# Kernel optimization log

Measured on AMD Instinct MI355X. Metric: run time of the kernel, lower is better.

Reference implementation:

```python
import jax, jax.numpy as jnp
import numpy as np
import math

B, TSRC, TTGT, DM, DI, H = 2, 2048, 2048, 1024, 1024, 16
DH = DI // H
LN_EPS = 1e-5


def setup_inputs() -> dict:
    key = jax.random.key(0)
    ks = iter(jax.random.split(key, 40))
    def p(*shape):
        return jax.random.normal(next(ks), shape, jnp.float32) * 0.02
    inp = {
        "enc_out_vecs": jax.random.normal(next(ks), (B, TSRC, DM), jnp.float32),
        "output_vecs": jax.random.normal(next(ks), (B, TTGT, DM), jnp.float32),
    }
    for tag in ("dd", "ed"):
        inp["Wq_" + tag] = p(DM, DI); inp["bq_" + tag] = jnp.zeros((DI,), jnp.float32)
        inp["Wk_" + tag] = p(DM, DI); inp["bk_" + tag] = jnp.zeros((DI,), jnp.float32)
        inp["Wv_" + tag] = p(DM, DI); inp["bv_" + tag] = jnp.zeros((DI,), jnp.float32)
        inp["Wo_" + tag] = p(DI, DM); inp["bo_" + tag] = jnp.zeros((DM,), jnp.float32)
        inp["W1_" + tag] = p(DM, 2 * DM); inp["b1_" + tag] = jnp.zeros((2 * DM,), jnp.float32)
        inp["W2_" + tag] = p(2 * DM, DM); inp["b2_" + tag] = jnp.zeros((DM,), jnp.float32)
        inp["g1_" + tag] = jnp.ones((DM,), jnp.float32); inp["be1_" + tag] = jnp.zeros((DM,), jnp.float32)
        inp["g2_" + tag] = jnp.ones((DM,), jnp.float32); inp["be2_" + tag] = jnp.zeros((DM,), jnp.float32)
    return inp


def _ln(x, g, b):
    m = jnp.mean(x, axis=-1, keepdims=True)
    v = jnp.var(x, axis=-1, keepdims=True)
    return (x - m) * jax.lax.rsqrt(v + LN_EPS) * g + b


def _mha(xq, xkv, Wq, bq, Wk, bk, Wv, bv, causal):
    Bb, Tq, _ = xq.shape
    Tk = xkv.shape[1]
    q = (xq @ Wq + bq).reshape(Bb, Tq, H, DH)
    k = (xkv @ Wk + bk).reshape(Bb, Tk, H, DH)
    v = (xkv @ Wv + bv).reshape(Bb, Tk, H, DH)
    s = jnp.einsum("bqhd,bkhd->bhqk", q, k) / math.sqrt(DH)
    if causal:
        mask = jnp.where(jnp.arange(Tk)[None, :] > jnp.arange(Tq)[:, None], -jnp.inf, 0.0)
        s = s + mask
    w = jax.nn.softmax(s, axis=-1)
    return jnp.einsum("bhqk,bkhd->bqhd", w, v).reshape(Bb, Tq, H * DH)


def reference(enc_out_vecs, output_vecs,
              Wq_dd, bq_dd, Wk_dd, bk_dd, Wv_dd, bv_dd, Wo_dd, bo_dd,
              W1_dd, b1_dd, W2_dd, b2_dd, g1_dd, be1_dd, g2_dd, be2_dd,
              Wq_ed, bq_ed, Wk_ed, bk_ed, Wv_ed, bv_ed, Wo_ed, bo_ed,
              W1_ed, b1_ed, W2_ed, b2_ed, g1_ed, be1_ed, g2_ed, be2_ed):
    # masked self-attention over decoder inputs
    x = output_vecs
    a = _mha(x, x, Wq_dd, bq_dd, Wk_dd, bk_dd, Wv_dd, bv_dd, causal=True)
    x = _ln(a @ Wo_dd + bo_dd + x, g1_dd, be1_dd)
    x = _ln(x + jax.nn.relu(x @ W1_dd + b1_dd) @ W2_dd + b2_dd, g2_dd, be2_dd)
    # cross attention against encoder outputs
    a = _mha(x, enc_out_vecs, Wq_ed, bq_ed, Wk_ed, bk_ed, Wv_ed, bv_ed, causal=False)
    x = _ln(a @ Wo_ed + bo_ed + x, g1_ed, be1_ed)
    x = _ln(jax.nn.relu(x @ W1_ed + b1_ed) @ W2_ed + b2_ed + x, g2_ed, be2_ed)
    return x
```

## Files before the change

kernel.cpp:

```cpp
#include <hip/hip_runtime.h>
#include <stdint.h>

#define DEV __device__ __forceinline__
typedef unsigned short u16;
typedef __attribute__((ext_vector_type(8))) short bf16x8;
typedef __attribute__((ext_vector_type(4))) float f32x4;

#define AS1 __attribute__((address_space(1)))
#define AS3 __attribute__((address_space(3)))
#define WAITVM0 asm volatile("s_waitcnt vmcnt(0)" ::: "memory")
#define QSCALE 0.18033688011112042f

DEV u16 f2bf(float f) {
  union { float f; uint32_t u; } x; x.f = f;
  uint32_t r = x.u + 0x7fffu + ((x.u >> 16) & 1u);
  return (u16)(r >> 16);
}

DEV uint32_t cvt_pk_bf16(float a, float b) {
  uint32_t r;
  asm("v_cvt_pk_bf16_f32 %0, %1, %2" : "=v"(r) : "v"(a), "v"(b));
  return r;
}

__global__ __launch_bounds__(256) void k_cvt2(const float* __restrict__ a, const float* __restrict__ bsrc,
                                              u16* __restrict__ oa, u16* __restrict__ ob, int n4) {
  int i = blockIdx.x * blockDim.x + threadIdx.x;
  const float* s;
  u16* o;
  int k;
  if (i < n4) { s = a; o = oa; k = i; }
  else        { s = bsrc; o = ob; k = i - n4; }
  float4 v = reinterpret_cast<const float4*>(s)[k];
  reinterpret_cast<ushort4*>(o)[k] = make_ushort4(f2bf(v.x), f2bf(v.y), f2bf(v.z), f2bf(v.w));
}

struct WTJob { const float* W; u16* WT; int K, M, msh, start; };
struct WTJobs { WTJob j[12]; };

__global__ void k_wT_all(WTJobs jobs) {
  __shared__ float tile[32][33];
  int b = blockIdx.x;
  int i = 0;
#pragma unroll
  for (int t = 1; t < 12; ++t)
    if (b >= jobs.j[t].start) i = t;
  const WTJob J = jobs.j[i];
  int rel = b - J.start;
  int m0 = (rel & ((1 << J.msh) - 1)) << 5;
  int k0 = (rel >> J.msh) << 5;
  int tx = threadIdx.x, ty = threadIdx.y;
#pragma unroll
  for (int q = 0; q < 4; ++q)
    tile[ty + q * 8][tx] = J.W[(size_t)(k0 + ty + q * 8) * J.M + m0 + tx];
  __syncthreads();
#pragma unroll
  for (int q = 0; q < 4; ++q)
    J.WT[(size_t)(m0 + ty + q * 8) * J.K + k0 + tx] = f2bf(tile[tx][ty + q * 8]);
}

template<int R>
DEV void stage_tile(const u16* __restrict__ g, int strideElems, u16* lds, int tid, int wv) {
#pragma unroll
  for (int t = 0; t < R / 32; ++t) {
    int idx = t * 256 + tid;
    int row = idx >> 3;
    int b = (idx & 7) << 4;
    int sb = b ^ ((row & 7) << 4);
    const char* src = (const char*)g + (size_t)row * strideElems * 2 + sb;
    char* dst = (char*)lds + (size_t)(t * 256 + wv * 64) * 16;
    __builtin_amdgcn_global_load_lds((const AS1 void*)src, (AS3 void*)dst, 16, 0, 0);
  }
}

DEV bf16x8 lds_frag(const u16* lds, int row, int kel) {
  int off = row * 128 + ((kel * 2) ^ ((row & 7) << 4));
  return *(const bf16x8*)((const char*)lds + off);
}

template<int JT, int MODE>
__global__ __launch_bounds__(256) void k_gemm(const u16* __restrict__ A, int lda,
                                              const u16* __restrict__ BT,
                                              const float* __restrict__ bias,
                                              void* __restrict__ C, int ldc, int K) {
  constexpr int BN = JT * 32;
  __shared__ __align__(16) u16 A_lds[2][128 * 64];
  __shared__ __align__(16) u16 B_lds[2][BN * 64];
  const int tid = threadIdx.x, lane = tid & 63, wv = tid >> 6;
  const int wm = wv >> 1, wn = wv & 1;
  const int nwg = gridDim.x * gridDim.y;
  const int flat = blockIdx.y * gridDim.x + blockIdx.x;
  const int sw = (flat & 7) * (nwg >> 3) + (flat >> 3);
  const int bx = sw % gridDim.x, by = sw / gridDim.x;
  const int bm0 = by * 128, bn0 = bx * BN;
  const int lr = lane & 15, lk = (lane >> 4) * 8, r0 = (lane >> 4) * 4;

  f32x4 acc[4][JT];
#pragma unroll
  for (int i = 0; i < 4; ++i)
#pragma unroll
    for (int j = 0; j < JT; ++j) acc[i][j] = f32x4{0.f, 0.f, 0.f, 0.f};

  stage_tile<128>(A + (size_t)bm0 * lda, lda, A_lds[0], tid, wv);
  stage_tile<BN>(BT + (size_t)bn0 * K, K, B_lds[0], tid, wv);
  WAITVM0;
  __builtin_amdgcn_s_barrier();

  int cur = 0;
  for (int k0 = 0; k0 < K; k0 += 64) {
    if (k0 + 64 < K) {
      stage_tile<128>(A + (size_t)bm0 * lda + k0 + 64, lda, A_lds[cur ^ 1], tid, wv);
      stage_tile<BN>(BT + (size_t)bn0 * K + k0 + 64, K, B_lds[cur ^ 1], tid, wv);
    }
#pragma unroll
    for (int kk = 0; kk < 2; ++kk) {
      bf16x8 af[4], bfr[JT];
#pragma unroll
      for (int i = 0; i < 4; ++i) af[i] = lds_frag(A_lds[cur], wm * 64 + i * 16 + lr, kk * 32 + lk);
#pragma unroll
      for (int j = 0; j < JT; ++j) bfr[j] = lds_frag(B_lds[cur], wn * (JT * 16) + j * 16 + lr, kk * 32 + lk);
#pragma unroll
      for (int i = 0; i < 4; ++i)
#pragma unroll
        for (int j = 0; j < JT; ++j)
          acc[i][j] = __builtin_amdgcn_mfma_f32_16x16x32_bf16(af[i], bfr[j], acc[i][j], 0, 0, 0);
    }
    WAITVM0;
    __builtin_amdgcn_s_barrier();
    cur ^= 1;
  }

#pragma unroll
  for (int j = 0; j < JT; ++j) {
    int col = bn0 + wn * (JT * 16) + j * 16 + lr;
    float bv = bias[col];
#pragma unroll
    for (int i = 0; i < 4; ++i) {
      int rowb = bm0 + wm * 64 + i * 16 + r0;
      if constexpr (MODE == 0) {
#pragma unroll
        for (int r = 0; r < 4; ++r)
          ((float*)C)[(size_t)(rowb + r) * ldc + col] = acc[i][j][r] + bv;
      } else {
#pragma unroll
        for (int r = 0; r < 4; ++r) {
          float v = fmaxf(acc[i][j][r] + bv, 0.f);
          ((u16*)C)[(size_t)(rowb + r) * ldc + col] = f2bf(v);
        }
      }
    }
  }
}

__global__ __launch_bounds__(256) void k_qkv(const u16* __restrict__ Aq, const u16* __restrict__ Akv,
                                             const u16* __restrict__ BT,
                                             const float* __restrict__ bq, const float* __restrict__ bk,
                                             const float* __restrict__ bv,
                                             u16* __restrict__ Qb, u16* __restrict__ Kb,
                                             u16* __restrict__ Vt, int K) {
  __shared__ __align__(16) u16 A_lds[2][128 * 64];
  __shared__ __align__(16) u16 B_lds[2][64 * 64];
  const int tid = threadIdx.x, lane = tid & 63, wv = tid >> 6;
  const int wm = wv >> 1, wn = wv & 1;
  const int nwg = gridDim.x * gridDim.y;
  const int flat = blockIdx.y * gridDim.x + blockIdx.x;
  const int sw = (flat & 7) * (nwg >> 3) + (flat >> 3);
  const int bx = sw % gridDim.x, by = sw / gridDim.x;
  const int bm0 = by * 128, bn0 = bx * 64;
  const int seg = bn0 >> 10;
  const u16* A = (seg == 0) ? Aq : Akv;
  const int lr = lane & 15, lk = (lane >> 4) * 8, r0 = (lane >> 4) * 4;

  f32x4 acc[4][2];
#pragma unroll
  for (int i = 0; i < 4; ++i)
#pragma unroll
    for (int j = 0; j < 2; ++j) acc[i][j] = f32x4{0.f, 0.f, 0.f, 0.f};

  stage_tile<128>(A + (size_t)bm0 * K, K, A_lds[0], tid, wv);
  stage_tile<64>(BT + (size_t)bn0 * K, K, B_lds[0], tid, wv);
  WAITVM0;
  __builtin_amdgcn_s_barrier();

  int cur = 0;
  for (int k0 = 0; k0 < K; k0 += 64) {
    if (k0 + 64 < K) {
      stage_tile<128>(A + (size_t)bm0 * K + k0 + 64, K, A_lds[cur ^ 1], tid, wv);
      stage_tile<64>(BT + (size_t)bn0 * K + k0 + 64, K, B_lds[cur ^ 1], tid, wv);
    }
#pragma unroll
    for (int kk = 0; kk < 2; ++kk) {
      bf16x8 af[4], bfr[2];
#pragma unroll
      for (int i = 0; i < 4; ++i) af[i] = lds_frag(A_lds[cur], wm * 64 + i * 16 + lr, kk * 32 + lk);
#pragma unroll
      for (int j = 0; j < 2; ++j) bfr[j] = lds_frag(B_lds[cur], wn * 32 + j * 16 + lr, kk * 32 + lk);
#pragma unroll
      for (int i = 0; i < 4; ++i)
#pragma unroll
        for (int j = 0; j < 2; ++j)
          acc[i][j] = __builtin_amdgcn_mfma_f32_16x16x32_bf16(af[i], bfr[j], acc[i][j], 0, 0, 0);
    }
    WAITVM0;
    __builtin_amdgcn_s_barrier();
    cur ^= 1;
  }

#pragma unroll
  for (int j = 0; j < 2; ++j) {
    int col = bn0 + wn * 32 + j * 16 + lr;
    int cl = col & 1023;
#pragma unroll
    for (int i = 0; i < 4; ++i) {
      int rowb = bm0 + wm * 64 + i * 16 + r0;
      if (seg == 0) {
        float bb = bq[cl];
#pragma unroll
        for (int r = 0; r < 4; ++r)
          Qb[(size_t)(rowb + r) * 1024 + cl] = f2bf((acc[i][j][r] + bb) * QSCALE);
      } else if (seg == 1) {
        float bb = bk[cl];
#pragma unroll
        for (int r = 0; r < 4; ++r)
          Kb[(size_t)(rowb + r) * 1024 + cl] = f2bf(acc[i][j][r] + bb);
      } else {
        float bb = bv[cl];
        int bidx = rowb >> 11, t = rowb & 2047;
        ushort4 o = make_ushort4(f2bf(acc[i][j][0] + bb), f2bf(acc[i][j][1] + bb),
                                 f2bf(acc[i][j][2] + bb), f2bf(acc[i][j][3] + bb));
        *reinterpret_cast<ushort4*>(&Vt[((size_t)bidx * 1024 + cl) * 2048 + t]) = o;
      }
    }
  }
}

__global__ __launch_bounds__(256) void k_ln(const float* __restrict__ Rm, const float* __restrict__ X,
                                            const float* __restrict__ g, const float* __restrict__ be,
                                            float* __restrict__ Y, u16* __restrict__ Yb) {
  int row = blockIdx.x;
  size_t base4 = (size_t)row * 256;
  int t = threadIdx.x;
  float4 a = reinterpret_cast<const float4*>(Rm)[base4 + t];
  float4 x = reinterpret_cast<const float4*>(X)[base4 + t];
  float v0 = a.x + x.x, v1 = a.y + x.y, v2 = a.z + x.z, v3 = a.w + x.w;
  float s = v0 + v1 + v2 + v3;
  float ss = v0 * v0 + v1 * v1 + v2 * v2 + v3 * v3;
#pragma unroll
  for (int m = 1; m < 64; m <<= 1) { s += __shfl_xor(s, m); ss += __shfl_xor(ss, m); }
  __shared__ float red[8];
  int wv = t >> 6;
  if ((t & 63) == 0) { red[wv] = s; red[4 + wv] = ss; }
  __syncthreads();
  s = red[0] + red[1] + red[2] + red[3];
  ss = red[4] + red[5] + red[6] + red[7];
  float mean = s * (1.f / 1024.f);
  float var = ss * (1.f / 1024.f) - mean * mean;
  float rstd = rsqrtf(var + 1e-5f);
  float4 gv = reinterpret_cast<const float4*>(g)[t];
  float4 bv = reinterpret_cast<const float4*>(be)[t];
  float o0 = (v0 - mean) * rstd * gv.x + bv.x;
  float o1 = (v1 - mean) * rstd * gv.y + bv.y;
  float o2 = (v2 - mean) * rstd * gv.z + bv.z;
  float o3 = (v3 - mean) * rstd * gv.w + bv.w;
  reinterpret_cast<float4*>(Y)[base4 + t] = make_float4(o0, o1, o2, o3);
  if (Yb) {
    ushort4 ob = make_ushort4(f2bf(o0), f2bf(o1), f2bf(o2), f2bf(o3));
    reinterpret_cast<ushort4*>(Yb)[base4 + t] = ob;
  }
}

template<bool CAUSAL>
__global__ __launch_bounds__(512) void k_attn(const u16* __restrict__ Q, const u16* __restrict__ Kg,
                                              const u16* __restrict__ Vt, u16* __restrict__ O,
                                              float* __restrict__ OP0, float* __restrict__ OP1,
                                              float* __restrict__ L0, float* __restrict__ L1, int T) {
  __shared__ __align__(16) u16 K_lds[3][64 * 64];
  __shared__ __align__(16) u16 V_lds[3][64 * 64];
  __shared__ __align__(16) u16 p_lds[8][16 * 64];
  const int tid = threadIdx.x, lane = tid & 63, wv = tid >> 6;
  const int h = blockIdx.y, b = blockIdx.z;
  const int lq = lane & 15, g = lane >> 4;
  const int swz = (lq & 7) << 4;
  const int fb0 = lq * 128 + ((g * 16) ^ swz);
  const int fb1 = lq * 128 + ((g * 16 + 64) ^ swz);
  const size_t qkbase = ((size_t)b * T) * 1024 + h * 64;
  const size_t vbase = ((size_t)b * 1024 + h * 64) * T;

  int qx, st, en;
  if constexpr (CAUSAL) {
    qx = 15 - (blockIdx.x >> 1);
    const int s = blockIdx.x & 1;
    const int ntf = 2 * qx + 2, half = qx + 1;
    st = s ? half : 0;
    en = s ? ntf : half;
  } else {
    qx = blockIdx.x;
    st = 0;
    en = T >> 6;
  }
  const int qw = qx * 128 + wv * 16;
  const int dtile = qw >> 6;

  bf16x8 aq0, aq1;
  {
    const u16* qp_ = Q + qkbase + (size_t)(qw + lq) * 1024 + g * 8;
    aq0 = *reinterpret_cast<const bf16x8*>(qp_);
    aq1 = *reinterpret_cast<const bf16x8*>(qp_ + 32);
  }

  const int srow = tid >> 3;
  const int ssb = ((tid & 7) << 4) ^ ((srow & 7) << 4);
  const char* ksrc = (const char*)(Kg + qkbase) + (size_t)srow * 2048 + ssb + (size_t)st * 131072;
  const char* vsrc = (const char*)(Vt + vbase) + (size_t)srow * ((size_t)T * 2) + ssb + (size_t)st * 128;
  const uint32_t doff = (uint32_t)(wv << 10);

  auto stage = [&](int buf) {
    __builtin_amdgcn_global_load_lds((const AS1 void*)ksrc, (AS3 void*)((char*)K_lds[buf] + doff), 16, 0, 0);
    __builtin_amdgcn_global_load_lds((const AS1 void*)vsrc, (AS3 void*)((char*)V_lds[buf] + doff), 16, 0, 0);
    ksrc += 131072;
    vsrc += 128;
  };

  f32x4 acc[4];
  float lsum = 0.f;
#pragma unroll
  for (int j = 0; j < 4; ++j) acc[j] = f32x4{0.f, 0.f, 0.f, 0.f};

  char* pw = (char*)p_lds[wv];

  auto qstep = [&](bool domask, int kv0, const char* kb, const char* vb) {
    f32x4 st_[4];
    __builtin_amdgcn_s_setprio(1);
#pragma unroll
    for (int j = 0; j < 4; ++j) {
      bf16x8 bk0 = *reinterpret_cast<const bf16x8*>(kb + fb0 + j * 2048);
      bf16x8 bk1 = *reinterpret_cast<const bf16x8*>(kb + fb1 + j * 2048);
      f32x4 t0 = f32x4{0.f, 0.f, 0.f, 0.f};
      t0 = __builtin_amdgcn_mfma_f32_16x16x32_bf16(bk0, aq0, t0, 0, 0, 0);
      t0 = __builtin_amdgcn_mfma_f32_16x16x32_bf16(bk1, aq1, t0, 0, 0, 0);
      st_[j] = t0;
    }
    __builtin_amdgcn_s_setprio(0);
    uint32_t pk[8];
    if (domask) {
      const int qrow = qw + lq;
#pragma unroll
      for (int j = 0; j < 4; ++j) {
        float p0 = __builtin_exp2f(st_[j][0]);
        float p1 = __builtin_exp2f(st_[j][1]);
        float p2 = __builtin_exp2f(st_[j][2]);
        float p3 = __builtin_exp2f(st_[j][3]);
        int kvb = kv0 + j * 16 + g * 4;
        p0 = (kvb > qrow) ? 0.f : p0;
        p1 = (kvb + 1 > qrow) ? 0.f : p1;
        p2 = (kvb + 2 > qrow) ? 0.f : p2;
        p3 = (kvb + 3 > qrow) ? 0.f : p3;
        lsum += (p0 + p1) + (p2 + p3);
        pk[2 * j] = cvt_pk_bf16(p0, p1);
        pk[2 * j + 1] = cvt_pk_bf16(p2, p3);
      }
    } else {
#pragma unroll
      for (int j = 0; j < 4; ++j) {
        float p0 = __builtin_exp2f(st_[j][0]);
        float p1 = __builtin_exp2f(st_[j][1]);
        float p2 = __builtin_exp2f(st_[j][2]);
        float p3 = __builtin_exp2f(st_[j][3]);
        lsum += (p0 + p1) + (p2 + p3);
        pk[2 * j] = cvt_pk_bf16(p0, p1);
        pk[2 * j + 1] = cvt_pk_bf16(p2, p3);
      }
    }
#pragma unroll
    for (int j = 0; j < 4; ++j)
      *reinterpret_cast<uint2*>(pw + lq * 128 + ((j * 32 + g * 8) ^ swz)) =
          make_uint2(pk[2 * j], pk[2 * j + 1]);
    bf16x8 pf0 = *reinterpret_cast<const bf16x8*>(pw + fb0);
    bf16x8 pf1 = *reinterpret_cast<const bf16x8*>(pw + fb1);
    __builtin_amdgcn_s_setprio(1);
#pragma unroll
    for (int j2 = 0; j2 < 4; ++j2) {
      bf16x8 v0 = *reinterpret_cast<const bf16x8*>(vb + fb0 + j2 * 2048);
      bf16x8 v1 = *reinterpret_cast<const bf16x8*>(vb + fb1 + j2 * 2048);
      acc[j2] = __builtin_amdgcn_mfma_f32_16x16x32_bf16(v0, pf0, acc[j2], 0, 0, 0);
      acc[j2] = __builtin_amdgcn_mfma_f32_16x16x32_bf16(v1, pf1, acc[j2], 0, 0, 0);
    }
    __builtin_amdgcn_s_setprio(0);
  };

  stage(0);
  if (st + 1 < en) {
    stage(1);
    asm volatile("s_waitcnt vmcnt(2)" ::: "memory");
  } else {
    WAITVM0;
  }
  __builtin_amdgcn_s_barrier();

  for (int it = st; it < en; ++it) {
    const int idx = it - st;
    if (it + 2 < en) stage((idx + 2) % 3);
    const char* kb = (const char*)K_lds[idx % 3];
    const char* vb = (const char*)V_lds[idx % 3];
    if (!CAUSAL || it <= dtile)
      qstep(CAUSAL && it == dtile, it << 6, kb, vb);
    if (it + 2 < en) {
      asm volatile("s_waitcnt vmcnt(2)" ::: "memory");
    } else {
      WAITVM0;
    }
    __builtin_amdgcn_s_barrier();
  }

  lsum += __shfl_xor(lsum, 16);
  lsum += __shfl_xor(lsum, 32);
  if constexpr (CAUSAL) {
    float* OP = (blockIdx.x & 1) ? OP1 : OP0;
    float* Lp = (blockIdx.x & 1) ? L1 : L0;
    const int row = (b * 16 + h) * 2048 + qw + lq;
    float* pr = OP + (size_t)row * 64;
#pragma unroll
    for (int j2 = 0; j2 < 4; ++j2)
      *reinterpret_cast<f32x4*>(pr + j2 * 16 + g * 4) = acc[j2];
    if (g == 0) Lp[row] = lsum;
  } else {
    float inv = 1.f / lsum;
    size_t rb = qkbase + (size_t)(qw + lq) * 1024;
#pragma unroll
    for (int j2 = 0; j2 < 4; ++j2) {
      ushort4 o = make_ushort4(f2bf(acc[j2][0] * inv), f2bf(acc[j2][1] * inv),
                               f2bf(acc[j2][2] * inv), f2bf(acc[j2][3] * inv));
      *reinterpret_cast<ushort4*>(&O[rb + j2 * 16 + g * 4]) = o;
    }
  }
}

__global__ __launch_bounds__(256) void k_amrg(const float* __restrict__ P0, const float* __restrict__ P1,
                                              const float* __restrict__ L0, const float* __restrict__ L1,
                                              u16* __restrict__ Ab) {
  int i = blockIdx.x * 256 + threadIdx.x;
  int row = i >> 4, d4 = (i & 15) << 2;
  f32x4 a = *reinterpret_cast<const f32x4*>(&P0[(size_t)row * 64 + d4]);
  f32x4 c = *reinterpret_cast<const f32x4*>(&P1[(size_t)row * 64 + d4]);
  float inv = 1.f / (L0[row] + L1[row]);
  int bh = row >> 11, q = row & 2047, bb = bh >> 4, hh = bh & 15;
  size_t dst = ((size_t)(bb * 2048 + q)) * 1024 + hh * 64 + d4;
  ushort4 o = make_ushort4(f2bf((a[0] + c[0]) * inv), f2bf((a[1] + c[1]) * inv),
                           f2bf((a[2] + c[2]) * inv), f2bf((a[3] + c[3]) * inv));
  *reinterpret_cast<ushort4*>(&Ab[dst]) = o;
}

extern "C" void kernel_launch(void* const* d_in, const int* in_sizes, int n_in,
                              void* d_out, int out_size, void* d_ws, size_t ws_size,
                              hipStream_t stream) {
  const int T = 2048;
  const float* enc = (const float*)d_in[0];
  const float* outv = (const float*)d_in[1];
  auto F = [&](int i) { return (const float*)d_in[i]; };

  size_t off = 0;
  auto alloc = [&](size_t bytes) {
    void* p = (char*)d_ws + off;
    off += (bytes + 255) & ~(size_t)255;
    return p;
  };

  const int tdK[12] = {1024, 1024, 1024, 1024, 1024, 2048, 1024, 1024, 1024, 1024, 1024, 2048};
  const int tdM[12] = {1024, 1024, 1024, 1024, 2048, 1024, 1024, 1024, 1024, 1024, 2048, 1024};
  const int tdIdx[12] = {2, 4, 6, 8, 10, 12, 18, 20, 22, 24, 26, 28};
  u16* WT_[12];
  for (int i = 0; i < 12; ++i) WT_[i] = (u16*)alloc((size_t)tdK[i] * tdM[i] * 2);

  u16* Xb0 = (u16*)alloc(4096ull * 1024 * 2);
  u16* Eb = (u16*)alloc(4096ull * 1024 * 2);
  u16* Qb = (u16*)alloc(4096ull * 1024 * 2);
  u16* Kb = (u16*)alloc(4096ull * 1024 * 2);
  u16* Vt = (u16*)alloc(4096ull * 1024 * 2);
  u16* Ab = (u16*)alloc(4096ull * 1024 * 2);
  u16* Hb = (u16*)alloc(4096ull * 2048 * 2);
  u16* Xbc = (u16*)alloc(4096ull * 1024 * 2);
  float* Rf = (float*)alloc(4096ull * 1024 * 4);
  float* Xfa = (float*)alloc(4096ull * 1024 * 4);
  float* Xfb = (float*)alloc(4096ull * 1024 * 4);
  float* Lsum = (float*)alloc(2ull * 65536 * 4);

  k_cvt2<<<8192, 256, 0, stream>>>(outv, enc, Xb0, Eb, 4096 * 1024 / 4);

  WTJobs jobs;
  int start = 0;
  for (int i = 0; i < 12; ++i) {
    int msh = (tdM[i] == 2048) ? 6 : 5;
    jobs.j[i] = {F(tdIdx[i]), WT_[i], tdK[i], tdM[i], msh, start};
    start += (tdM[i] >> 5) * (tdK[i] >> 5);
  }
  k_wT_all<<<start, dim3(32, 8), 0, stream>>>(jobs);

  float* OP0 = Rf;
  float* OP1 = (float*)Hb;
  float* L0 = Lsum;
  float* L1 = Lsum + 65536;

  dim3 gq(48, 32);
  dim3 g1k(16, 32);
  dim3 g2k(16, 32);
  dim3 gac(32, 16, 2);
  dim3 gan(16, 16, 2);

  k_qkv<<<gq, 256, 0, stream>>>(Xb0, Xb0, WT_[0], F(3), F(5), F(7), Qb, Kb, Vt, 1024);
  k_attn<true><<<gac, 512, 0, stream>>>(Qb, Kb, Vt, Ab, OP0, OP1, L0, L1, T);
  k_amrg<<<4096, 256, 0, stream>>>(OP0, OP1, L0, L1, Ab);
  k_gemm<2, 0><<<g1k, 256, 0, stream>>>(Ab, 1024, WT_[3], F(9), Rf, 1024, 1024);
  k_ln<<<4096, 256, 0, stream>>>(Rf, outv, F(14), F(15), Xfa, Xbc);
  k_gemm<4, 2><<<g2k, 256, 0, stream>>>(Xbc, 1024, WT_[4], F(11), Hb, 2048, 1024);
  k_gemm<2, 0><<<g1k, 256, 0, stream>>>(Hb, 2048, WT_[5], F(13), Rf, 1024, 2048);
  k_ln<<<4096, 256, 0, stream>>>(Rf, Xfa, F(16), F(17), Xfb, Xbc);

  k_qkv<<<gq, 256, 0, stream>>>(Xbc, Eb, WT_[6], F(19), F(21), F(23), Qb, Kb, Vt, 1024);
  k_attn<false><<<gan, 512, 0, stream>>>(Qb, Kb, Vt, Ab, OP0, OP1, L0, L1, T);
  k_gemm<2, 0><<<g1k, 256, 0, stream>>>(Ab, 1024, WT_[9], F(25), Rf, 1024, 1024);
  k_ln<<<4096, 256, 0, stream>>>(Rf, Xfb, F(30), F(31), Xfa, Xbc);
  k_gemm<4, 2><<<g2k, 256, 0, stream>>>(Xbc, 1024, WT_[10], F(27), Hb, 2048, 1024);
  k_gemm<2, 0><<<g1k, 256, 0, stream>>>(Hb, 2048, WT_[11], F(29), Rf, 1024, 2048);
  k_ln<<<4096, 256, 0, stream>>>(Rf, Xfa, F(32), F(33), (float*)d_out, (u16*)nullptr);
}
```

Before: 444.5 us.

## Use 4-wave attention blocks with 32 query rows per wave, drop causal split-KV merge

The attention kernel now runs 256-thread blocks where each wave handles two 16-row query tiles, so every K/V fragment read from LDS feeds twice as many MFMAs. Each thread issues two async loads per tensor per stage to keep the 64x64 K/V tiles filled. The causal path no longer splits the KV range across two blocks with fp32 partial outputs and a separate merge kernel. Instead each block walks the whole causal range and writes normalized bf16 directly, removing the merge launch and its partial-result traffic. The trade-off is fewer blocks in flight for the causal pass, more load imbalance between long and short query tiles, and higher register pressure per wave.

```diff
diff --git a/kernel.cpp b/kernel.cpp
--- a/kernel.cpp
+++ b/kernel.cpp
@@ -270,13 +270,11 @@
 }
 
 template<bool CAUSAL>
-__global__ __launch_bounds__(512) void k_attn(const u16* __restrict__ Q, const u16* __restrict__ Kg,
-                                              const u16* __restrict__ Vt, u16* __restrict__ O,
-                                              float* __restrict__ OP0, float* __restrict__ OP1,
-                                              float* __restrict__ L0, float* __restrict__ L1, int T) {
+__global__ __launch_bounds__(256) void k_attn(const u16* __restrict__ Q, const u16* __restrict__ Kg,
+                                              const u16* __restrict__ Vt, u16* __restrict__ O, int T) {
   __shared__ __align__(16) u16 K_lds[3][64 * 64];
   __shared__ __align__(16) u16 V_lds[3][64 * 64];
-  __shared__ __align__(16) u16 p_lds[8][16 * 64];
+  __shared__ __align__(16) u16 p_lds[4][32 * 64];
   const int tid = threadIdx.x, lane = tid & 63, wv = tid >> 6;
   const int h = blockIdx.y, b = blockIdx.z;
   const int lq = lane & 15, g = lane >> 4;
@@ -286,168 +284,164 @@
   const size_t qkbase = ((size_t)b * T) * 1024 + h * 64;
   const size_t vbase = ((size_t)b * 1024 + h * 64) * T;
 
-  int qx, st, en;
-  if constexpr (CAUSAL) {
-    qx = 15 - (blockIdx.x >> 1);
-    const int s = blockIdx.x & 1;
-    const int ntf = 2 * qx + 2, half = qx + 1;
-    st = s ? half : 0;
-    en = s ? ntf : half;
-  } else {
-    qx = blockIdx.x;
-    st = 0;
-    en = T >> 6;
-  }
-  const int qw = qx * 128 + wv * 16;
+  const int qx = CAUSAL ? (gridDim.x - 1 - blockIdx.x) : blockIdx.x;
+  const int en = CAUSAL ? (2 * qx + 2) : (T >> 6);
+  const int qw = qx * 128 + wv * 32;
   const int dtile = qw >> 6;
 
-  bf16x8 aq0, aq1;
-  {
-    const u16* qp_ = Q + qkbase + (size_t)(qw + lq) * 1024 + g * 8;
-    aq0 = *reinterpret_cast<const bf16x8*>(qp_);
-    aq1 = *reinterpret_cast<const bf16x8*>(qp_ + 32);
+  bf16x8 aq[2][2];
+#pragma unroll
+  for (int i0 = 0; i0 < 2; ++i0) {
+    const u16* qp_ = Q + qkbase + (size_t)(qw + i0 * 16 + lq) * 1024 + g * 8;
+    aq[i0][0] = *reinterpret_cast<const bf16x8*>(qp_);
+    aq[i0][1] = *reinterpret_cast<const bf16x8*>(qp_ + 32);
   }
 
   const int srow = tid >> 3;
   const int ssb = ((tid & 7) << 4) ^ ((srow & 7) << 4);
-  const char* ksrc = (const char*)(Kg + qkbase) + (size_t)srow * 2048 + ssb + (size_t)st * 131072;
-  const char* vsrc = (const char*)(Vt + vbase) + (size_t)srow * ((size_t)T * 2) + ssb + (size_t)st * 128;
-  const uint32_t doff = (uint32_t)(wv << 10);
+  const char* ksrc = (const char*)(Kg + qkbase) + (size_t)srow * 2048 + ssb;
+  const char* vsrc = (const char*)(Vt + vbase) + (size_t)srow * ((size_t)T * 2) + ssb;
+  const int vstep2 = T * 64;
+  const uint32_t doff = (uint32_t)((tid & 192) << 4);
 
   auto stage = [&](int buf) {
-    __builtin_amdgcn_global_load_lds((const AS1 void*)ksrc, (AS3 void*)((char*)K_lds[buf] + doff), 16, 0, 0);
-    __builtin_amdgcn_global_load_lds((const AS1 void*)vsrc, (AS3 void*)((char*)V_lds[buf] + doff), 16, 0, 0);
+    char* kd = (char*)K_lds[buf] + doff;
+    char* vd = (char*)V_lds[buf] + doff;
+    __builtin_amdgcn_global_load_lds((const AS1 void*)ksrc, (AS3 void*)kd, 16, 0, 0);
+    __builtin_amdgcn_global_load_lds((const AS1 void*)(ksrc + 65536), (AS3 void*)(kd + 4096), 16, 0, 0);
+    __builtin_amdgcn_global_load_lds((const AS1 void*)vsrc, (AS3 void*)vd, 16, 0, 0);
+    __builtin_amdgcn_global_load_lds((const AS1 void*)(vsrc + vstep2), (AS3 void*)(vd + 4096), 16, 0, 0);
     ksrc += 131072;
     vsrc += 128;
   };
 
-  f32x4 acc[4];
-  float lsum = 0.f;
-#pragma unroll
-  for (int j = 0; j < 4; ++j) acc[j] = f32x4{0.f, 0.f, 0.f, 0.f};
+  f32x4 acc[2][4];
+  float lsum[2] = {0.f, 0.f};
+#pragma unroll
+  for (int i0 = 0; i0 < 2; ++i0)
+#pragma unroll
+    for (int j = 0; j < 4; ++j) acc[i0][j] = f32x4{0.f, 0.f, 0.f, 0.f};
 
   char* pw = (char*)p_lds[wv];
 
   auto qstep = [&](bool domask, int kv0, const char* kb, const char* vb) {
-    f32x4 st_[4];
+    f32x4 s0[4], s1[4];
     __builtin_amdgcn_s_setprio(1);
 #pragma unroll
     for (int j = 0; j < 4; ++j) {
       bf16x8 bk0 = *reinterpret_cast<const bf16x8*>(kb + fb0 + j * 2048);
       bf16x8 bk1 = *reinterpret_cast<const bf16x8*>(kb + fb1 + j * 2048);
       f32x4 t0 = f32x4{0.f, 0.f, 0.f, 0.f};
-      t0 = __builtin_amdgcn_mfma_f32_16x16x32_bf16(bk0, aq0, t0, 0, 0, 0);
-      t0 = __builtin_amdgcn_mfma_f32_16x16x32_bf16(bk1, aq1, t0, 0, 0, 0);
-      st_[j] = t0;
+      t0 = __builtin_amdgcn_mfma_f32_16x16x32_bf16(bk0, aq[0][0], t0, 0, 0, 0);
+      t0 = __builtin_amdgcn_mfma_f32_16x16x32_bf16(bk1, aq[0][1], t0, 0, 0, 0);
+      s0[j] = t0;
+      f32x4 t1 = f32x4{0.f, 0.f, 0.f, 0.f};
+      t1 = __builtin_amdgcn_mfma_f32_16x16x32_bf16(bk0, aq[1][0], t1, 0, 0, 0);
+      t1 = __builtin_amdgcn_mfma_f32_16x16x32_bf16(bk1, aq[1][1], t1, 0, 0, 0);
+      s1[j] = t1;
     }
     __builtin_amdgcn_s_setprio(0);
-    uint32_t pk[8];
+    uint32_t pk0[8], pk1[8];
     if (domask) {
-      const int qrow = qw + lq;
+      const int q0r = qw + lq, q1r = qw + 16 + lq;
 #pragma unroll
       for (int j = 0; j < 4; ++j) {
-        float p0 = __builtin_exp2f(st_[j][0]);
-        float p1 = __builtin_exp2f(st_[j][1]);
-        float p2 = __builtin_exp2f(st_[j][2]);
-        float p3 = __builtin_exp2f(st_[j][3]);
         int kvb = kv0 + j * 16 + g * 4;
-        p0 = (kvb > qrow) ? 0.f : p0;
-        p1 = (kvb + 1 > qrow) ? 0.f : p1;
-        p2 = (kvb + 2 > qrow) ? 0.f : p2;
-        p3 = (kvb + 3 > qrow) ? 0.f : p3;
-        lsum += (p0 + p1) + (p2 + p3);
-        pk[2 * j] = cvt_pk_bf16(p0, p1);
-        pk[2 * j + 1] = cvt_pk_bf16(p2, p3);
+        float a0 = __builtin_exp2f(s0[j][0]), a1 = __builtin_exp2f(s0[j][1]);
+        float a2 = __builtin_exp2f(s0[j][2]), a3 = __builtin_exp2f(s0[j][3]);
+        a0 = (kvb > q0r) ? 0.f : a0;
+        a1 = (kvb + 1 > q0r) ? 0.f : a1;
+        a2 = (kvb + 2 > q0r) ? 0.f : a2;
+        a3 = (kvb + 3 > q0r) ? 0.f : a3;
+        lsum[0] += (a0 + a1) + (a2 + a3);
+        pk0[2 * j] = cvt_pk_bf16(a0, a1);
+        pk0[2 * j + 1] = cvt_pk_bf16(a2, a3);
+        float c0 = __builtin_exp2f(s1[j][0]), c1 = __builtin_exp2f(s1[j][1]);
+        float c2 = __builtin_exp2f(s1[j][2]), c3 = __builtin_exp2f(s1[j][3]);
+        c0 = (kvb > q1r) ? 0.f : c0;
+        c1 = (kvb + 1 > q1r) ? 0.f : c1;
+        c2 = (kvb + 2 > q1r) ? 0.f : c2;
+        c3 = (kvb + 3 > q1r) ? 0.f : c3;
+        lsum[1] += (c0 + c1) + (c2 + c3);
+        pk1[2 * j] = cvt_pk_bf16(c0, c1);
+        pk1[2 * j + 1] = cvt_pk_bf16(c2, c3);
       }
     } else {
 #pragma unroll
       for (int j = 0; j < 4; ++j) {
-        float p0 = __builtin_exp2f(st_[j][0]);
-        float p1 = __builtin_exp2f(st_[j][1]);
-        float p2 = __builtin_exp2f(st_[j][2]);
-        float p3 = __builtin_exp2f(st_[j][3]);
-        lsum += (p0 + p1) + (p2 + p3);
-        pk[2 * j] = cvt_pk_bf16(p0, p1);
-        pk[2 * j + 1] = cvt_pk_bf16(p2, p3);
+        float a0 = __builtin_exp2f(s0[j][0]), a1 = __builtin_exp2f(s0[j][1]);
+        float a2 = __builtin_exp2f(s0[j][2]), a3 = __builtin_exp2f(s0[j][3]);
+        lsum[0] += (a0 + a1) + (a2 + a3);
+        pk0[2 * j] = cvt_pk_bf16(a0, a1);
+        pk0[2 * j + 1] = cvt_pk_bf16(a2, a3);
+        float c0 = __builtin_exp2f(s1[j][0]), c1 = __builtin_exp2f(s1[j][1]);
+        float c2 = __builtin_exp2f(s1[j][2]), c3 = __builtin_exp2f(s1[j][3]);
+        lsum[1] += (c0 + c1) + (c2 + c3);
+        pk1[2 * j] = cvt_pk_bf16(c0, c1);
+        pk1[2 * j + 1] = cvt_pk_bf16(c2, c3);
       }
     }
 #pragma unroll
-    for (int j = 0; j < 4; ++j)
+    for (int j = 0; j < 4; ++j) {
       *reinterpret_cast<uint2*>(pw + lq * 128 + ((j * 32 + g * 8) ^ swz)) =
-          make_uint2(pk[2 * j], pk[2 * j + 1]);
-    bf16x8 pf0 = *reinterpret_cast<const bf16x8*>(pw + fb0);
-    bf16x8 pf1 = *reinterpret_cast<const bf16x8*>(pw + fb1);
+          make_uint2(pk0[2 * j], pk0[2 * j + 1]);
+      *reinterpret_cast<uint2*>(pw + 2048 + lq * 128 + ((j * 32 + g * 8) ^ swz)) =
+          make_uint2(pk1[2 * j], pk1[2 * j + 1]);
+    }
+    bf16x8 pf00 = *reinterpret_cast<const bf16x8*>(pw + fb0);
+    bf16x8 pf01 = *reinterpret_cast<const bf16x8*>(pw + fb1);
+    bf16x8 pf10 = *reinterpret_cast<const bf16x8*>(pw + 2048 + fb0);
+    bf16x8 pf11 = *reinterpret_cast<const bf16x8*>(pw + 2048 + fb1);
     __builtin_amdgcn_s_setprio(1);
 #pragma unroll
     for (int j2 = 0; j2 < 4; ++j2) {
       bf16x8 v0 = *reinterpret_cast<const bf16x8*>(vb + fb0 + j2 * 2048);
       bf16x8 v1 = *reinterpret_cast<const bf16x8*>(vb + fb1 + j2 * 2048);
-      acc[j2] = __builtin_amdgcn_mfma_f32_16x16x32_bf16(v0, pf0, acc[j2], 0, 0, 0);
-      acc[j2] = __builtin_amdgcn_mfma_f32_16x16x32_bf16(v1, pf1, acc[j2], 0, 0, 0);
+      acc[0][j2] = __builtin_amdgcn_mfma_f32_16x16x32_bf16(v0, pf00, acc[0][j2], 0, 0, 0);
+      acc[0][j2] = __builtin_amdgcn_mfma_f32_16x16x32_bf16(v1, pf01, acc[0][j2], 0, 0, 0);
+      acc[1][j2] = __builtin_amdgcn_mfma_f32_16x16x32_bf16(v0, pf10, acc[1][j2], 0, 0, 0);
+      acc[1][j2] = __builtin_amdgcn_mfma_f32_16x16x32_bf16(v1, pf11, acc[1][j2], 0, 0, 0);
     }
     __builtin_amdgcn_s_setprio(0);
   };
 
   stage(0);
-  if (st + 1 < en) {
+  if (en > 1) {
     stage(1);
-    asm volatile("s_waitcnt vmcnt(2)" ::: "memory");
+    asm volatile("s_waitcnt vmcnt(4)" ::: "memory");
   } else {
     WAITVM0;
   }
   __builtin_amdgcn_s_barrier();
 
-  for (int it = st; it < en; ++it) {
-    const int idx = it - st;
-    if (it + 2 < en) stage((idx + 2) % 3);
-    const char* kb = (const char*)K_lds[idx % 3];
-    const char* vb = (const char*)V_lds[idx % 3];
+  for (int it = 0; it < en; ++it) {
+    if (it + 2 < en) stage((it + 2) % 3);
+    const char* kb = (const char*)K_lds[it % 3];
+    const char* vb = (const char*)V_lds[it % 3];
     if (!CAUSAL || it <= dtile)
       qstep(CAUSAL && it == dtile, it << 6, kb, vb);
     if (it + 2 < en) {
-      asm volatile("s_waitcnt vmcnt(2)" ::: "memory");
+      asm volatile("s_waitcnt vmcnt(4)" ::: "memory");
     } else {
       WAITVM0;
     }
     __builtin_amdgcn_s_barrier();
   }
 
-  lsum += __shfl_xor(lsum, 16);
-  lsum += __shfl_xor(lsum, 32);
-  if constexpr (CAUSAL) {
-    float* OP = (blockIdx.x & 1) ? OP1 : OP0;
-    float* Lp = (blockIdx.x & 1) ? L1 : L0;
-    const int row = (b * 16 + h) * 2048 + qw + lq;
-    float* pr = OP + (size_t)row * 64;
-#pragma unroll
-    for (int j2 = 0; j2 < 4; ++j2)
-      *reinterpret_cast<f32x4*>(pr + j2 * 16 + g * 4) = acc[j2];
-    if (g == 0) Lp[row] = lsum;
-  } else {
-    float inv = 1.f / lsum;
-    size_t rb = qkbase + (size_t)(qw + lq) * 1024;
+#pragma unroll
+  for (int i0 = 0; i0 < 2; ++i0) {
+    float ls = lsum[i0];
+    ls += __shfl_xor(ls, 16);
+    ls += __shfl_xor(ls, 32);
+    float inv = 1.f / ls;
+    size_t rb = qkbase + (size_t)(qw + i0 * 16 + lq) * 1024;
 #pragma unroll
     for (int j2 = 0; j2 < 4; ++j2) {
-      ushort4 o = make_ushort4(f2bf(acc[j2][0] * inv), f2bf(acc[j2][1] * inv),
-                               f2bf(acc[j2][2] * inv), f2bf(acc[j2][3] * inv));
+      ushort4 o = make_ushort4(f2bf(acc[i0][j2][0] * inv), f2bf(acc[i0][j2][1] * inv),
+                               f2bf(acc[i0][j2][2] * inv), f2bf(acc[i0][j2][3] * inv));
       *reinterpret_cast<ushort4*>(&O[rb + j2 * 16 + g * 4]) = o;
     }
   }
-}
-
-__global__ __launch_bounds__(256) void k_amrg(const float* __restrict__ P0, const float* __restrict__ P1,
-                                              const float* __restrict__ L0, const float* __restrict__ L1,
-                                              u16* __restrict__ Ab) {
-  int i = blockIdx.x * 256 + threadIdx.x;
-  int row = i >> 4, d4 = (i & 15) << 2;
-  f32x4 a = *reinterpret_cast<const f32x4*>(&P0[(size_t)row * 64 + d4]);
-  f32x4 c = *reinterpret_cast<const f32x4*>(&P1[(size_t)row * 64 + d4]);
-  float inv = 1.f / (L0[row] + L1[row]);
-  int bh = row >> 11, q = row & 2047, bb = bh >> 4, hh = bh & 15;
-  size_t dst = ((size_t)(bb * 2048 + q)) * 1024 + hh * 64 + d4;
-  ushort4 o = make_ushort4(f2bf((a[0] + c[0]) * inv), f2bf((a[1] + c[1]) * inv),
-                           f2bf((a[2] + c[2]) * inv), f2bf((a[3] + c[3]) * inv));
-  *reinterpret_cast<ushort4*>(&Ab[dst]) = o;
 }
 
 extern "C" void kernel_launch(void* const* d_in, const int* in_sizes, int n_in,
@@ -482,7 +476,6 @@
   float* Rf = (float*)alloc(4096ull * 1024 * 4);
   float* Xfa = (float*)alloc(4096ull * 1024 * 4);
   float* Xfb = (float*)alloc(4096ull * 1024 * 4);
-  float* Lsum = (float*)alloc(2ull * 65536 * 4);
 
   k_cvt2<<<8192, 256, 0, stream>>>(outv, enc, Xb0, Eb, 4096 * 1024 / 4);
 
@@ -495,20 +488,13 @@
   }
   k_wT_all<<<start, dim3(32, 8), 0, stream>>>(jobs);
 
-  float* OP0 = Rf;
-  float* OP1 = (float*)Hb;
-  float* L0 = Lsum;
-  float* L1 = Lsum + 65536;
-
   dim3 gq(48, 32);
   dim3 g1k(16, 32);
   dim3 g2k(16, 32);
-  dim3 gac(32, 16, 2);
-  dim3 gan(16, 16, 2);
+  dim3 ga(16, 16, 2);
 
   k_qkv<<<gq, 256, 0, stream>>>(Xb0, Xb0, WT_[0], F(3), F(5), F(7), Qb, Kb, Vt, 1024);
-  k_attn<true><<<gac, 512, 0, stream>>>(Qb, Kb, Vt, Ab, OP0, OP1, L0, L1, T);
-  k_amrg<<<4096, 256, 0, stream>>>(OP0, OP1, L0, L1, Ab);
+  k_attn<true><<<ga, 256, 0, stream>>>(Qb, Kb, Vt, Ab, T);
   k_gemm<2, 0><<<g1k, 256, 0, stream>>>(Ab, 1024, WT_[3], F(9), Rf, 1024, 1024);
   k_ln<<<4096, 256, 0, stream>>>(Rf, outv, F(14), F(15), Xfa, Xbc);
   k_gemm<4, 2><<<g2k, 256, 0, stream>>>(Xbc, 1024, WT_[4], F(11), Hb, 2048, 1024);
@@ -516,10 +502,10 @@
   k_ln<<<4096, 256, 0, stream>>>(Rf, Xfa, F(16), F(17), Xfb, Xbc);
 
   k_qkv<<<gq, 256, 0, stream>>>(Xbc, Eb, WT_[6], F(19), F(21), F(23), Qb, Kb, Vt, 1024);
-  k_attn<false><<<gan, 512, 0, stream>>>(Qb, Kb, Vt, Ab, OP0, OP1, L0, L1, T);
+  k_attn<false><<<ga, 256, 0, stream>>>(Qb, Kb, Vt, Ab, T);
   k_gemm<2, 0><<<g1k, 256, 0, stream>>>(Ab, 1024, WT_[9], F(25), Rf, 1024, 1024);
   k_ln<<<4096, 256, 0, stream>>>(Rf, Xfb, F(30), F(31), Xfa, Xbc);
   k_gemm<4, 2><<<g2k, 256, 0, stream>>>(Xbc, 1024, WT_[10], F(27), Hb, 2048, 1024);
-  k_gemm<2, 0><<<g1k, 256, 0, stream>>>(Hb, 2048, WT_[11], F(29), Rf, 1024, 2048);
+  k_gemm<2, 0><<<g1k, 256, 0, stream>>>(Hb, 2048, WT_[5 + 6], F(29), Rf, 1024, 2048);
   k_ln<<<4096, 256, 0, stream>>>(Rf, Xfa, F(32), F(33), (float*)d_out, (u16*)nullptr);
 }
```

Result: slower. 454.2 us (+2.2%).

## Use 512-thread 256x64 GEMM tiles sharing the B tile across eight waves

Applied to the files above, without the earlier changes.

The GEMM and QKV kernels now run with 512 threads (8 waves) and cover a 256-row by 64-column output tile, so each staged B tile is shared by twice as many rows. The loader is rewritten to issue loads across all 512 threads, the templated wide-N variant for the FFN up-projection is dropped in favour of 64-wide tiles with twice as many columns of blocks, and the grids are halved in M. The aim is to cut redundant B-tile global traffic and raise MFMA work per barrier. In exchange, LDS use per block grows and the block count halves (256 or 512 blocks), which may leave compute units underfilled or lower occupancy.

```diff
diff --git a/kernel.cpp b/kernel.cpp
--- a/kernel.cpp
+++ b/kernel.cpp
@@ -60,15 +60,15 @@
 }
 
 template<int R>
-DEV void stage_tile(const u16* __restrict__ g, int strideElems, u16* lds, int tid, int wv) {
-#pragma unroll
-  for (int t = 0; t < R / 32; ++t) {
-    int idx = t * 256 + tid;
+DEV void stage512(const u16* __restrict__ g, int strideElems, u16* lds, int tid, int wv) {
+#pragma unroll
+  for (int t = 0; t < R / 64; ++t) {
+    int idx = t * 512 + tid;
     int row = idx >> 3;
     int b = (idx & 7) << 4;
     int sb = b ^ ((row & 7) << 4);
     const char* src = (const char*)g + (size_t)row * strideElems * 2 + sb;
-    char* dst = (char*)lds + (size_t)(t * 256 + wv * 64) * 16;
+    char* dst = (char*)lds + (size_t)(t * 512 + wv * 64) * 16;
     __builtin_amdgcn_global_load_lds((const AS1 void*)src, (AS3 void*)dst, 16, 0, 0);
   }
 }
@@ -78,87 +78,12 @@
   return *(const bf16x8*)((const char*)lds + off);
 }
 
-template<int JT, int MODE>
-__global__ __launch_bounds__(256) void k_gemm(const u16* __restrict__ A, int lda,
+template<int MODE>
+__global__ __launch_bounds__(512) void k_gemm(const u16* __restrict__ A, int lda,
                                               const u16* __restrict__ BT,
                                               const float* __restrict__ bias,
                                               void* __restrict__ C, int ldc, int K) {
-  constexpr int BN = JT * 32;
-  __shared__ __align__(16) u16 A_lds[2][128 * 64];
-  __shared__ __align__(16) u16 B_lds[2][BN * 64];
-  const int tid = threadIdx.x, lane = tid & 63, wv = tid >> 6;
-  const int wm = wv >> 1, wn = wv & 1;
-  const int nwg = gridDim.x * gridDim.y;
-  const int flat = blockIdx.y * gridDim.x + blockIdx.x;
-  const int sw = (flat & 7) * (nwg >> 3) + (flat >> 3);
-  const int bx = sw % gridDim.x, by = sw / gridDim.x;
-  const int bm0 = by * 128, bn0 = bx * BN;
-  const int lr = lane & 15, lk = (lane >> 4) * 8, r0 = (lane >> 4) * 4;
-
-  f32x4 acc[4][JT];
-#pragma unroll
-  for (int i = 0; i < 4; ++i)
-#pragma unroll
-    for (int j = 0; j < JT; ++j) acc[i][j] = f32x4{0.f, 0.f, 0.f, 0.f};
-
-  stage_tile<128>(A + (size_t)bm0 * lda, lda, A_lds[0], tid, wv);
-  stage_tile<BN>(BT + (size_t)bn0 * K, K, B_lds[0], tid, wv);
-  WAITVM0;
-  __builtin_amdgcn_s_barrier();
-
-  int cur = 0;
-  for (int k0 = 0; k0 < K; k0 += 64) {
-    if (k0 + 64 < K) {
-      stage_tile<128>(A + (size_t)bm0 * lda + k0 + 64, lda, A_lds[cur ^ 1], tid, wv);
-      stage_tile<BN>(BT + (size_t)bn0 * K + k0 + 64, K, B_lds[cur ^ 1], tid, wv);
-    }
-#pragma unroll
-    for (int kk = 0; kk < 2; ++kk) {
-      bf16x8 af[4], bfr[JT];
-#pragma unroll
-      for (int i = 0; i < 4; ++i) af[i] = lds_frag(A_lds[cur], wm * 64 + i * 16 + lr, kk * 32 + lk);
-#pragma unroll
-      for (int j = 0; j < JT; ++j) bfr[j] = lds_frag(B_lds[cur], wn * (JT * 16) + j * 16 + lr, kk * 32 + lk);
-#pragma unroll
-      for (int i = 0; i < 4; ++i)
-#pragma unroll
-        for (int j = 0; j < JT; ++j)
-          acc[i][j] = __builtin_amdgcn_mfma_f32_16x16x32_bf16(af[i], bfr[j], acc[i][j], 0, 0, 0);
-    }
-    WAITVM0;
-    __builtin_amdgcn_s_barrier();
-    cur ^= 1;
-  }
-
-#pragma unroll
-  for (int j = 0; j < JT; ++j) {
-    int col = bn0 + wn * (JT * 16) + j * 16 + lr;
-    float bv = bias[col];
-#pragma unroll
-    for (int i = 0; i < 4; ++i) {
-      int rowb = bm0 + wm * 64 + i * 16 + r0;
-      if constexpr (MODE == 0) {
-#pragma unroll
-        for (int r = 0; r < 4; ++r)
-          ((float*)C)[(size_t)(rowb + r) * ldc + col] = acc[i][j][r] + bv;
-      } else {
-#pragma unroll
-        for (int r = 0; r < 4; ++r) {
-          float v = fmaxf(acc[i][j][r] + bv, 0.f);
-          ((u16*)C)[(size_t)(rowb + r) * ldc + col] = f2bf(v);
-        }
-      }
-    }
-  }
-}
-
-__global__ __launch_bounds__(256) void k_qkv(const u16* __restrict__ Aq, const u16* __restrict__ Akv,
-                                             const u16* __restrict__ BT,
-                                             const float* __restrict__ bq, const float* __restrict__ bk,
-                                             const float* __restrict__ bv,
-                                             u16* __restrict__ Qb, u16* __restrict__ Kb,
-                                             u16* __restrict__ Vt, int K) {
-  __shared__ __align__(16) u16 A_lds[2][128 * 64];
+  __shared__ __align__(16) u16 A_lds[2][256 * 64];
   __shared__ __align__(16) u16 B_lds[2][64 * 64];
   const int tid = threadIdx.x, lane = tid & 63, wv = tid >> 6;
   const int wm = wv >> 1, wn = wv & 1;
@@ -166,7 +91,81 @@
   const int flat = blockIdx.y * gridDim.x + blockIdx.x;
   const int sw = (flat & 7) * (nwg >> 3) + (flat >> 3);
   const int bx = sw % gridDim.x, by = sw / gridDim.x;
-  const int bm0 = by * 128, bn0 = bx * 64;
+  const int bm0 = by * 256, bn0 = bx * 64;
+  const int lr = lane & 15, lk = (lane >> 4) * 8, r0 = (lane >> 4) * 4;
+
+  f32x4 acc[4][2];
+#pragma unroll
+  for (int i = 0; i < 4; ++i)
+#pragma unroll
+    for (int j = 0; j < 2; ++j) acc[i][j] = f32x4{0.f, 0.f, 0.f, 0.f};
+
+  stage512<256>(A + (size_t)bm0 * lda, lda, A_lds[0], tid, wv);
+  stage512<64>(BT + (size_t)bn0 * K, K, B_lds[0], tid, wv);
+  WAITVM0;
+  __builtin_amdgcn_s_barrier();
+
+  int cur = 0;
+  for (int k0 = 0; k0 < K; k0 += 64) {
+    if (k0 + 64 < K) {
+      stage512<256>(A + (size_t)bm0 * lda + k0 + 64, lda, A_lds[cur ^ 1], tid, wv);
+      stage512<64>(BT + (size_t)bn0 * K + k0 + 64, K, B_lds[cur ^ 1], tid, wv);
+    }
+#pragma unroll
+    for (int kk = 0; kk < 2; ++kk) {
+      bf16x8 af[4], bfr[2];
+#pragma unroll
+      for (int i = 0; i < 4; ++i) af[i] = lds_frag(A_lds[cur], wm * 64 + i * 16 + lr, kk * 32 + lk);
+#pragma unroll
+      for (int j = 0; j < 2; ++j) bfr[j] = lds_frag(B_lds[cur], wn * 32 + j * 16 + lr, kk * 32 + lk);
+#pragma unroll
+      for (int i = 0; i < 4; ++i)
+#pragma unroll
+        for (int j = 0; j < 2; ++j)
+          acc[i][j] = __builtin_amdgcn_mfma_f32_16x16x32_bf16(af[i], bfr[j], acc[i][j], 0, 0, 0);
+    }
+    WAITVM0;
+    __builtin_amdgcn_s_barrier();
+    cur ^= 1;
+  }
+
+#pragma unroll
+  for (int j = 0; j < 2; ++j) {
+    int col = bn0 + wn * 32 + j * 16 + lr;
+    float bv = bias[col];
+#pragma unroll
+    for (int i = 0; i < 4; ++i) {
+      int rowb = bm0 + wm * 64 + i * 16 + r0;
+      if constexpr (MODE == 0) {
+#pragma unroll
+        for (int r = 0; r < 4; ++r)
+          ((float*)C)[(size_t)(rowb + r) * ldc + col] = acc[i][j][r] + bv;
+      } else {
+#pragma unroll
+        for (int r = 0; r < 4; ++r) {
+          float v = fmaxf(acc[i][j][r] + bv, 0.f);
+          ((u16*)C)[(size_t)(rowb + r) * ldc + col] = f2bf(v);
+        }
+      }
+    }
+  }
+}
+
+__global__ __launch_bounds__(512) void k_qkv(const u16* __restrict__ Aq, const u16* __restrict__ Akv,
+                                             const u16* __restrict__ BT,
+                                             const float* __restrict__ bq, const float* __restrict__ bk,
+                                             const float* __restrict__ bv,
+                                             u16* __restrict__ Qb, u16* __restrict__ Kb,
+                                             u16* __restrict__ Vt, int K) {
+  __shared__ __align__(16) u16 A_lds[2][256 * 64];
+  __shared__ __align__(16) u16 B_lds[2][64 * 64];
+  const int tid = threadIdx.x, lane = tid & 63, wv = tid >> 6;
+  const int wm = wv >> 1, wn = wv & 1;
+  const int nwg = gridDim.x * gridDim.y;
+  const int flat = blockIdx.y * gridDim.x + blockIdx.x;
+  const int sw = (flat & 7) * (nwg >> 3) + (flat >> 3);
+  const int bx = sw % gridDim.x, by = sw / gridDim.x;
+  const int bm0 = by * 256, bn0 = bx * 64;
   const int seg = bn0 >> 10;
   const u16* A = (seg == 0) ? Aq : Akv;
   const int lr = lane & 15, lk = (lane >> 4) * 8, r0 = (lane >> 4) * 4;
@@ -177,16 +176,16 @@
 #pragma unroll
     for (int j = 0; j < 2; ++j) acc[i][j] = f32x4{0.f, 0.f, 0.f, 0.f};
 
-  stage_tile<128>(A + (size_t)bm0 * K, K, A_lds[0], tid, wv);
-  stage_tile<64>(BT + (size_t)bn0 * K, K, B_lds[0], tid, wv);
+  stage512<256>(A + (size_t)bm0 * K, K, A_lds[0], tid, wv);
+  stage512<64>(BT + (size_t)bn0 * K, K, B_lds[0], tid, wv);
   WAITVM0;
   __builtin_amdgcn_s_barrier();
 
   int cur = 0;
   for (int k0 = 0; k0 < K; k0 += 64) {
     if (k0 + 64 < K) {
-      stage_tile<128>(A + (size_t)bm0 * K + k0 + 64, K, A_lds[cur ^ 1], tid, wv);
-      stage_tile<64>(BT + (size_t)bn0 * K + k0 + 64, K, B_lds[cur ^ 1], tid, wv);
+      stage512<256>(A + (size_t)bm0 * K + k0 + 64, K, A_lds[cur ^ 1], tid, wv);
+      stage512<64>(BT + (size_t)bn0 * K + k0 + 64, K, B_lds[cur ^ 1], tid, wv);
     }
 #pragma unroll
     for (int kk = 0; kk < 2; ++kk) {
@@ -500,26 +499,26 @@
   float* L0 = Lsum;
   float* L1 = Lsum + 65536;
 
-  dim3 gq(48, 32);
-  dim3 g1k(16, 32);
-  dim3 g2k(16, 32);
+  dim3 gq(48, 16);
+  dim3 g1k(16, 16);
+  dim3 g2k(32, 16);
   dim3 gac(32, 16, 2);
   dim3 gan(16, 16, 2);
 
-  k_qkv<<<gq, 256, 0, stream>>>(Xb0, Xb0, WT_[0], F(3), F(5), F(7), Qb, Kb, Vt, 1024);
+  k_qkv<<<gq, 512, 0, stream>>>(Xb0, Xb0, WT_[0], F(3), F(5), F(7), Qb, Kb, Vt, 1024);
   k_attn<true><<<gac, 512, 0, stream>>>(Qb, Kb, Vt, Ab, OP0, OP1, L0, L1, T);
   k_amrg<<<4096, 256, 0, stream>>>(OP0, OP1, L0, L1, Ab);
-  k_gemm<2, 0><<<g1k, 256, 0, stream>>>(Ab, 1024, WT_[3], F(9), Rf, 1024, 1024);
+  k_gemm<0><<<g1k, 512, 0, stream>>>(Ab, 1024, WT_[3], F(9), Rf, 1024, 1024);
   k_ln<<<4096, 256, 0, stream>>>(Rf, outv, F(14), F(15), Xfa, Xbc);
-  k_gemm<4, 2><<<g2k, 256, 0, stream>>>(Xbc, 1024, WT_[4], F(11), Hb, 2048, 1024);
-  k_gemm<2, 0><<<g1k, 256, 0, stream>>>(Hb, 2048, WT_[5], F(13), Rf, 1024, 2048);
+  k_gemm<2><<<g2k, 512, 0, stream>>>(Xbc, 1024, WT_[4], F(11), Hb, 2048, 1024);
+  k_gemm<0><<<g1k, 512, 0, stream>>>(Hb, 2048, WT_[5], F(13), Rf, 1024, 2048);
   k_ln<<<4096, 256, 0, stream>>>(Rf, Xfa, F(16), F(17), Xfb, Xbc);
 
-  k_qkv<<<gq, 256, 0, stream>>>(Xbc, Eb, WT_[6], F(19), F(21), F(23), Qb, Kb, Vt, 1024);
+  k_qkv<<<gq, 512, 0, stream>>>(Xbc, Eb, WT_[6], F(19), F(21), F(23), Qb, Kb, Vt, 1024);
   k_attn<false><<<gan, 512, 0, stream>>>(Qb, Kb, Vt, Ab, OP0, OP1, L0, L1, T);
-  k_gemm<2, 0><<<g1k, 256, 0, stream>>>(Ab, 1024, WT_[9], F(25), Rf, 1024, 1024);
+  k_gemm<0><<<g1k, 512, 0, stream>>>(Ab, 1024, WT_[9], F(25), Rf, 1024, 1024);
   k_ln<<<4096, 256, 0, stream>>>(Rf, Xfb, F(30), F(31), Xfa, Xbc);
-  k_gemm<4, 2><<<g2k, 256, 0, stream>>>(Xbc, 1024, WT_[10], F(27), Hb, 2048, 1024);
-  k_gemm<2, 0><<<g1k, 256, 0, stream>>>(Hb, 2048, WT_[11], F(29), Rf, 1024, 2048);
+  k_gemm<2><<<g2k, 512, 0, stream>>>(Xbc, 1024, WT_[10], F(27), Hb, 2048, 1024);
+  k_gemm<0><<<g1k, 512, 0, stream>>>(Hb, 2048, WT_[11], F(29), Rf, 1024, 2048);
   k_ln<<<4096, 256, 0, stream>>>(Rf, Xfa, F(32), F(33), (float*)d_out, (u16*)nullptr);
 }
```

After: 458.9 us. +3.2%, slower.
